# Kernel optimization log

Measured on AMD Instinct MI355X. Metric: run time of the kernel, lower is better.

## Reference

```python
import jax, jax.numpy as jnp
import numpy as np

VOCAB = 32
UTT_LEN = 16
NUM_MEANING_TYPES = 5
MEANINGS_PER_TYPE = 10
SUPPORT_SIZE = 100000  # = MEANINGS_PER_TYPE ** NUM_MEANING_TYPES
BATCH = 2048


def setup_inputs() -> dict:
    key = jax.random.key(0)
    k1, k2, k3 = jax.random.split(key, 3)
    # query utterances: [utt_len, batch] token ids
    utts = jax.random.randint(k1, (UTT_LEN, BATCH), 0, VOCAB, dtype=jnp.int64)
    # support set is stored as one-hot encoded utterances [S, utt_len*vocab]
    support_tokens = jax.random.randint(k2, (SUPPORT_SIZE, UTT_LEN), 0, VOCAB)
    support = jax.nn.one_hot(support_tokens, VOCAB, dtype=jnp.float32)
    support = support.reshape(SUPPORT_SIZE, UTT_LEN * VOCAB)
    # meanings table [S, num_meaning_types]
    meanings_t = jax.random.randint(k3, (SUPPORT_SIZE, NUM_MEANING_TYPES), 0,
                                    MEANINGS_PER_TYPE, dtype=jnp.int64)
    return {"utts": utts, "support": support, "meanings_t": meanings_t}


def reference(utts, support, meanings_t):
    # utts: [M, N] ints; support: [S, M*V] floats; meanings_t: [S, T] ints
    M, N = utts.shape
    # one-hot encode queries: [N, M, V] -> [N, M*V]
    batch_fluffy = jax.nn.one_hot(utts.T, VOCAB, dtype=jnp.float32).reshape(N, M * VOCAB)
    batch_sq = jnp.sum(batch_fluffy * batch_fluffy, axis=1)        # [N]
    support_sq = jnp.sum(support * support, axis=1)                # [S]
    cross = batch_fluffy @ support.T                                # [N, S]
    squared_dist = batch_sq[:, None] + support_sq[None, :] - 2.0 * cross
    # top-1 smallest distance (K=1)
    top1 = jnp.argmin(squared_dist, axis=1)                         # [N]
    meanings = meanings_t[top1]                                     # [N, T]
    return jax.nn.one_hot(meanings, MEANINGS_PER_TYPE, dtype=jnp.float32)
```

## Files before the change

### kernel.cpp

```cpp
#include <hip/hip_runtime.h>
#include <stdint.h>

#define S_ROWS 100000
#define NQ     2048
#define M_POS  16
#define VOCABS 32
#define WPB    8
#define GROUPS 8
#define CHUNKS 125
#define RC     800
#define KITER  25

__global__ __launch_bounds__(256) void knn_decode(const float* __restrict__ support,
                                                  uint8_t* __restrict__ tok) {
    int wave = (blockIdx.x * 256 + threadIdx.x) >> 6;
    int lane = threadIdx.x & 63;
    if (wave >= S_ROWS) return;
    const float4* rowp = (const float4*)(support + (size_t)wave * 512) + lane * 2;
    float4 f0 = rowp[0];
    float4 f1 = rowp[1];
    float base = (float)((lane & 3) * 64);
    float v = f0.x * (base + 0.f)  + f0.y * (base + 8.f)  + f0.z * (base + 16.f) + f0.w * (base + 24.f)
            + f1.x * (base + 32.f) + f1.y * (base + 40.f) + f1.z * (base + 48.f) + f1.w * (base + 56.f);
    v += __shfl_xor(v, 1);
    v += __shfl_xor(v, 2);
    if ((lane & 3) == 0) {
        int p = lane >> 2;
        tok[(size_t)wave * 16 + p] = (uint8_t)(v + 0.5f);
    }
}

__device__ __forceinline__ void FA(uint32_t a, uint32_t b, uint32_t c,
                                   uint32_t& s, uint32_t& co) {
    uint32_t x = a ^ b;
    s  = x ^ c;
    co = (a & b) | (x & c);
}
__device__ __forceinline__ void HA(uint32_t a, uint32_t b, uint32_t& s, uint32_t& co) {
    s = a ^ b; co = a & b;
}

__global__ __launch_bounds__(256) void knn_score(const int* __restrict__ utts,
                                                 const uint8_t* __restrict__ tok,
                                                 uint32_t* __restrict__ gkeys) {
    __shared__ uint32_t table[M_POS * VOCABS * WPB];
    __shared__ uint32_t lkeys[256];

    const int bid = blockIdx.x;
    const int g   = bid & 7;
    const int c   = bid >> 3;
    const int t   = threadIdx.x;

    #pragma unroll
    for (int i = 0; i < 16; ++i) table[t + 256 * i] = 0u;
    lkeys[t] = 0u;
    __syncthreads();

    {
        int q = g * 256 + t;
        int wb = t >> 5, j = t & 31;
        #pragma unroll
        for (int m = 0; m < M_POS; ++m) {
            int v = utts[m * NQ + q];
            atomicOr(&table[(m * VOCABS + v) * WPB + wb], 1u << j);
        }
    }
    __syncthreads();

    const int w   = t & 7;
    const int sub = t >> 3;
    const int r0  = c * RC;
    const uint32_t* tw = table + w;

    uint32_t cp0=0,cp1=0,cp2=0,cp3=0,cp4=0;
    uint32_t k0p=0,k1p=0,k2p=0,k3p=0,k4p=0;

    for (int k = 0; k < KITER; ++k) {
        int s = r0 + sub + 32 * k;
        const uint4* tp = (const uint4*)(tok + (size_t)s * 16);
        uint4 ta = tp[0];
        uint32_t b[16];
        b[0]  = tw[ (ta.x        & 0xFFu) +  0*256];
        b[1]  = tw[((ta.x >> 8)  & 0xFFu) +  1*256];
        b[2]  = tw[((ta.x >> 16) & 0xFFu) +  2*256];
        b[3]  = tw[((ta.x >> 24)        ) +  3*256];
        b[4]  = tw[ (ta.y        & 0xFFu) +  4*256];
        b[5]  = tw[((ta.y >> 8)  & 0xFFu) +  5*256];
        b[6]  = tw[((ta.y >> 16) & 0xFFu) +  6*256];
        b[7]  = tw[((ta.y >> 24)        ) +  7*256];
        b[8]  = tw[ (ta.z        & 0xFFu) +  8*256];
        b[9]  = tw[((ta.z >> 8)  & 0xFFu) +  9*256];
        b[10] = tw[((ta.z >> 16) & 0xFFu) + 10*256];
        b[11] = tw[((ta.z >> 24)        ) + 11*256];
        b[12] = tw[ (ta.w        & 0xFFu) + 12*256];
        b[13] = tw[((ta.w >> 8)  & 0xFFu) + 13*256];
        b[14] = tw[((ta.w >> 16) & 0xFFu) + 14*256];
        b[15] = tw[((ta.w >> 24)        ) + 15*256];

        uint32_t s10,s11,s12,s13,s14, c10,c11,c12,c13,c14;
        FA(b[0],b[1],b[2],   s10,c10);
        FA(b[3],b[4],b[5],   s11,c11);
        FA(b[6],b[7],b[8],   s12,c12);
        FA(b[9],b[10],b[11], s13,c13);
        FA(b[12],b[13],b[14],s14,c14);
        uint32_t s2a,c2a,s2b,c2b;
        FA(s10,s11,s12, s2a,c2a);
        FA(s13,s14,b[15], s2b,c2b);
        uint32_t n0,h0;  HA(s2a,s2b, n0,h0);
        uint32_t u,cu,vv,cv,x2,cx,n1,cy;
        FA(c10,c11,c12, u,cu);
        FA(c13,c14,c2a, vv,cv);
        FA(u,vv,c2b,    x2,cx);
        HA(x2,h0,       n1,cy);
        uint32_t y4,cz,n2,cw,n3,n4;
        FA(cu,cv,cx, y4,cz);
        HA(y4,cy,    n2,cw);
        HA(cz,cw,    n3,n4);

        uint32_t eq = ~(n4 ^ cp4);
        uint32_t gt = n4 & ~cp4;
        gt |= eq & (n3 & ~cp3);  eq &= ~(n3 ^ cp3);
        gt |= eq & (n2 & ~cp2);  eq &= ~(n2 ^ cp2);
        gt |= eq & (n1 & ~cp1);  eq &= ~(n1 ^ cp1);
        gt |= eq & (n0 & ~cp0);

        uint32_t ng = ~gt;
        cp0 = (gt & n0) | (ng & cp0);
        cp1 = (gt & n1) | (ng & cp1);
        cp2 = (gt & n2) | (ng & cp2);
        cp3 = (gt & n3) | (ng & cp3);
        cp4 = (gt & n4) | (ng & cp4);
        uint32_t m0 = 0u - (uint32_t)( k       & 1);
        uint32_t m1 = 0u - (uint32_t)((k >> 1) & 1);
        uint32_t m2 = 0u - (uint32_t)((k >> 2) & 1);
        uint32_t m3 = 0u - (uint32_t)((k >> 3) & 1);
        uint32_t m4 = 0u - (uint32_t)((k >> 4) & 1);
        k0p = (gt & m0) | (ng & k0p);
        k1p = (gt & m1) | (ng & k1p);
        k2p = (gt & m2) | (ng & k2p);
        k3p = (gt & m3) | (ng & k3p);
        k4p = (gt & m4) | (ng & k4p);
    }

    #pragma unroll 1
    for (int j = 0; j < 32; ++j) {
        uint32_t cnt = ((cp0>>j)&1u) | (((cp1>>j)&1u)<<1) | (((cp2>>j)&1u)<<2)
                     | (((cp3>>j)&1u)<<3) | (((cp4>>j)&1u)<<4);
        uint32_t kk  = ((k0p>>j)&1u) | (((k1p>>j)&1u)<<1) | (((k2p>>j)&1u)<<2)
                     | (((k3p>>j)&1u)<<3) | (((k4p>>j)&1u)<<4);
        uint32_t idx = (uint32_t)(r0 + sub) + 32u * kk;
        uint32_t key = (cnt << 17) | (0x1FFFFu - idx);
        atomicMax(&lkeys[w * 32 + j], key);
    }
    __syncthreads();
    atomicMax(&gkeys[g * 256 + t], lkeys[t]);
}

__global__ __launch_bounds__(256) void knn_out(const uint32_t* __restrict__ gkeys,
                                               const int* __restrict__ meanings,
                                               float* __restrict__ out) {
    int n = blockIdx.x * 256 + threadIdx.x;
    if (n >= NQ) return;
    uint32_t key = gkeys[n];
    int idx = 0x1FFFF - (int)(key & 0x1FFFFu);
    float* o = out + (size_t)n * 50;
    #pragma unroll
    for (int tt = 0; tt < 5; ++tt) {
        int mv = meanings[(size_t)idx * 5 + tt];
        #pragma unroll
        for (int mm = 0; mm < 10; ++mm) o[tt * 10 + mm] = (mm == mv) ? 1.0f : 0.0f;
    }
}

extern "C" void kernel_launch(void* const* d_in, const int* in_sizes, int n_in,
                              void* d_out, int out_size, void* d_ws, size_t ws_size,
                              hipStream_t stream) {
    const int*   utts     = (const int*)d_in[0];
    const float* support  = (const float*)d_in[1];
    const int*   meanings = (const int*)d_in[2];
    float* out = (float*)d_out;

    uint8_t*  tok   = (uint8_t*)d_ws;
    uint32_t* gkeys = (uint32_t*)((char*)d_ws + (size_t)S_ROWS * 16);

    hipMemsetAsync(gkeys, 0, NQ * sizeof(uint32_t), stream);
    knn_decode<<<(S_ROWS + 3) / 4, 256, 0, stream>>>(support, tok);
    knn_score<<<GROUPS * CHUNKS, 256, 0, stream>>>(utts, tok, gkeys);
    knn_out<<<NQ / 256, 256, 0, stream>>>(gkeys, meanings, out);
}
```

Measured before the change: 325.4 us.

## Replace atomic top-1 reduction with shared-memory transpose and partial-buffer reduce

The per-block argmax reduction no longer issues 32 serialized LDS atomicMax calls per thread followed by global atomicMax. Each thread now writes its 32 keys into a padded shared array, and each thread then reduces one query across the 32 subgroups. Per-chunk results go to a partial buffer that the final kernel reduces over 125 chunks before emitting the one-hot output. This also removes the memset, but it adds 1 MB of partial-buffer traffic, a serial 125-iteration loop in a kernel of only 8 blocks, and about 33 KB of extra shared memory that may lower occupancy.

```diff
diff --git a/kernel.cpp b/kernel.cpp
--- a/kernel.cpp
+++ b/kernel.cpp
@@ -10,6 +10,7 @@
 #define CHUNKS 125
 #define RC     800
 #define KITER  25
+#define KPAD   264
 
 __global__ __launch_bounds__(256) void knn_decode(const float* __restrict__ support,
                                                   uint8_t* __restrict__ tok) {
@@ -42,9 +43,9 @@
 
 __global__ __launch_bounds__(256) void knn_score(const int* __restrict__ utts,
                                                  const uint8_t* __restrict__ tok,
-                                                 uint32_t* __restrict__ gkeys) {
+                                                 uint32_t* __restrict__ partial) {
     __shared__ uint32_t table[M_POS * VOCABS * WPB];
-    __shared__ uint32_t lkeys[256];
+    __shared__ uint32_t keys[32 * KPAD];
 
     const int bid = blockIdx.x;
     const int g   = bid & 7;
@@ -53,7 +54,6 @@
 
     #pragma unroll
     for (int i = 0; i < 16; ++i) table[t + 256 * i] = 0u;
-    lkeys[t] = 0u;
     __syncthreads();
 
     {
@@ -142,28 +142,46 @@
         k4p = (gt & m4) | (ng & k4p);
     }
 
-    #pragma unroll 1
-    for (int j = 0; j < 32; ++j) {
-        uint32_t cnt = ((cp0>>j)&1u) | (((cp1>>j)&1u)<<1) | (((cp2>>j)&1u)<<2)
-                     | (((cp3>>j)&1u)<<3) | (((cp4>>j)&1u)<<4);
-        uint32_t kk  = ((k0p>>j)&1u) | (((k1p>>j)&1u)<<1) | (((k2p>>j)&1u)<<2)
-                     | (((k3p>>j)&1u)<<3) | (((k4p>>j)&1u)<<4);
-        uint32_t idx = (uint32_t)(r0 + sub) + 32u * kk;
-        uint32_t key = (cnt << 17) | (0x1FFFFu - idx);
-        atomicMax(&lkeys[w * 32 + j], key);
+    {
+        uint32_t C = 0x1FFFFu - (uint32_t)(r0 + sub);
+        #pragma unroll
+        for (int j = 0; j < 32; ++j) {
+            uint32_t cnt = ((cp0>>j)&1u) | (((cp1>>j)&1u)<<1) | (((cp2>>j)&1u)<<2)
+                         | (((cp3>>j)&1u)<<3) | (((cp4>>j)&1u)<<4);
+            uint32_t kk  = ((k0p>>j)&1u) | (((k1p>>j)&1u)<<1) | (((k2p>>j)&1u)<<2)
+                         | (((k3p>>j)&1u)<<3) | (((k4p>>j)&1u)<<4);
+            uint32_t key = (cnt << 17) + C - (kk << 5);
+            keys[j * KPAD + t] = key;
+        }
     }
     __syncthreads();
-    atomicMax(&gkeys[g * 256 + t], lkeys[t]);
-}
-
-__global__ __launch_bounds__(256) void knn_out(const uint32_t* __restrict__ gkeys,
-                                               const int* __restrict__ meanings,
-                                               float* __restrict__ out) {
-    int n = blockIdx.x * 256 + threadIdx.x;
-    if (n >= NQ) return;
-    uint32_t key = gkeys[n];
-    int idx = 0x1FFFF - (int)(key & 0x1FFFFu);
-    float* o = out + (size_t)n * 50;
+
+    {
+        int w2 = t & 7, j2 = t >> 3;
+        const uint32_t* kp = keys + j2 * KPAD + w2;
+        uint32_t best = 0;
+        #pragma unroll
+        for (int i = 0; i < 32; ++i) {
+            uint32_t v = kp[8 * i];
+            best = best > v ? best : v;
+        }
+        partial[(size_t)c * NQ + g * 256 + w2 * 32 + j2] = best;
+    }
+}
+
+__global__ __launch_bounds__(256) void knn_reduce_out(const uint32_t* __restrict__ partial,
+                                                      const int* __restrict__ meanings,
+                                                      float* __restrict__ out) {
+    int q = blockIdx.x * 256 + threadIdx.x;
+    if (q >= NQ) return;
+    uint32_t best = 0;
+    #pragma unroll 5
+    for (int c = 0; c < CHUNKS; ++c) {
+        uint32_t v = partial[(size_t)c * NQ + q];
+        best = best > v ? best : v;
+    }
+    int idx = 0x1FFFF - (int)(best & 0x1FFFFu);
+    float* o = out + (size_t)q * 50;
     #pragma unroll
     for (int tt = 0; tt < 5; ++tt) {
         int mv = meanings[(size_t)idx * 5 + tt];
@@ -180,11 +198,10 @@
     const int*   meanings = (const int*)d_in[2];
     float* out = (float*)d_out;
 
-    uint8_t*  tok   = (uint8_t*)d_ws;
-    uint32_t* gkeys = (uint32_t*)((char*)d_ws + (size_t)S_ROWS * 16);
-
-    hipMemsetAsync(gkeys, 0, NQ * sizeof(uint32_t), stream);
+    uint8_t*  tok     = (uint8_t*)d_ws;
+    uint32_t* partial = (uint32_t*)((char*)d_ws + (size_t)S_ROWS * 16);
+
     knn_decode<<<(S_ROWS + 3) / 4, 256, 0, stream>>>(support, tok);
-    knn_score<<<GROUPS * CHUNKS, 256, 0, stream>>>(utts, tok, gkeys);
-    knn_out<<<NQ / 256, 256, 0, stream>>>(gkeys, meanings, out);
-}
+    knn_score<<<GROUPS * CHUNKS, 256, 0, stream>>>(utts, tok, partial);
+    knn_reduce_out<<<NQ / 256, 256, 0, stream>>>(partial, meanings, out);
+}
```

After: 332.8 us. 2.3% more time.
